# Kernel optimization log

Hardware: AMD Instinct MI355X
Metric: run time of the kernel (lower is better)

The kernel has to match this reference:

```python
import jax, jax.numpy as jnp
import numpy as np
from jax import lax

C = 128
G = 8          # deformable groups
K = 3
KK = K * K
PAD = 1


def conv2d(x, w, pad):
    return lax.conv_general_dilated(
        x, w, window_strides=(1, 1), padding=((pad, pad), (pad, pad)),
        dimension_numbers=('NCHW', 'OIHW', 'NCHW'))


def deform_conv_v2(x, offset, mask, weight, bias):
    """Modulated deformable conv (DCNv2), stride=1, pad=1, dil=1.
    x:[B,C,H,W] offset:[B,2*G*KK,H,W] mask:[B,G*KK,H,W] weight:[O,C,K,K]."""
    B, Cin, H, W = x.shape
    Cg = Cin // G
    # CUDA kernel layout per group: [k0_y, k0_x, k1_y, k1_x, ...]
    off = offset.reshape(B, G, KK, 2, H, W)
    off_y, off_x = off[:, :, :, 0], off[:, :, :, 1]          # [B,G,KK,H,W]
    m = mask.reshape(B, G, KK, H, W)

    kyy, kxx = jnp.meshgrid(jnp.arange(K), jnp.arange(K), indexing='ij')
    kyy = kyy.reshape(KK).astype(x.dtype)
    kxx = kxx.reshape(KK).astype(x.dtype)
    yy = jnp.arange(H, dtype=x.dtype)
    xx = jnp.arange(W, dtype=x.dtype)
    # absolute sampling positions [B,G,KK,H,W]
    py = yy[None, None, None, :, None] - PAD + kyy[None, None, :, None, None] + off_y
    px = xx[None, None, None, None, :] - PAD + kxx[None, None, :, None, None] + off_x

    y0 = jnp.floor(py)
    x0 = jnp.floor(px)
    ly = py - y0
    lx = px - x0

    xg = x.reshape(B, G, Cg, H * W)

    def gather(yi, xi):
        valid = ((yi >= 0) & (yi <= H - 1) & (xi >= 0) & (xi <= W - 1)).astype(x.dtype)
        yc = jnp.clip(yi, 0, H - 1).astype(jnp.int32)
        xc = jnp.clip(xi, 0, W - 1).astype(jnp.int32)
        idx = (yc * W + xc).reshape(B, G, 1, KK * H * W)
        v = jnp.take_along_axis(xg, idx, axis=3).reshape(B, G, Cg, KK, H, W)
        return v * valid[:, :, None]

    val = (gather(y0, x0) * ((1 - ly) * (1 - lx))[:, :, None]
           + gather(y0, x0 + 1) * ((1 - ly) * lx)[:, :, None]
           + gather(y0 + 1, x0) * (ly * (1 - lx))[:, :, None]
           + gather(y0 + 1, x0 + 1) * (ly * lx)[:, :, None])
    val = val * m[:, :, None]                                # modulation

    w = weight.reshape(-1, G, Cg, KK)                        # [O,G,Cg,KK]
    out = jnp.einsum('bgckhw,ogck->bohw', val, w)
    return out + bias[None, :, None, None]


def setup_inputs() -> dict:
    key = jax.random.key(0)
    ks = jax.random.split(key, 7)
    B, H, W = 4, 128, 128
    feat_l = jax.random.normal(ks[0], (B, C, H, W), jnp.float32)
    feat_s = jax.random.normal(ks[1], (B, C, H // 2, W // 2), jnp.float32)
    # 1x1 offset conv (256 -> 128), bias=False
    W_off = jax.random.normal(ks[2], (C, 2 * C, 1, 1), jnp.float32) * (1.0 / np.sqrt(2 * C))
    # conv_offset_mask: 128 -> G*3*KK = 216, 3x3, bias=True (zero-init in practice; small random here)
    W_om = jax.random.normal(ks[3], (G * 3 * KK, C, K, K), jnp.float32) * 0.01
    b_om = jax.random.normal(ks[4], (G * 3 * KK,), jnp.float32) * 0.01
    # DCN weight 128 -> 128, 3x3
    W_dcn = jax.random.normal(ks[5], (C, C, K, K), jnp.float32) * (1.0 / np.sqrt(C * KK))
    b_dcn = jax.random.normal(ks[6], (C,), jnp.float32) * 0.01
    return {'feat_l': feat_l, 'feat_s': feat_s, 'W_off': W_off,
            'W_om': W_om, 'b_om': b_om, 'W_dcn': W_dcn, 'b_dcn': b_dcn}


def reference(feat_l, feat_s, W_off, W_om, b_om, W_dcn, b_dcn):
    B, Cc, H, W = feat_l.shape
    # F.interpolate bilinear align_corners=False == jax.image.resize bilinear
    feat_up = jax.image.resize(feat_s, (B, Cc, H, W), method='bilinear')
    offset_feat = conv2d(jnp.concatenate([feat_l, feat_up * 2], axis=1), W_off, pad=0)
    om = conv2d(offset_feat, W_om, pad=1) + b_om[None, :, None, None]
    o1, o2, mask = jnp.split(om, 3, axis=1)
    offset = jnp.concatenate([o1, o2], axis=1)
    mask = jax.nn.sigmoid(mask)
    feat_align = jax.nn.relu(deform_conv_v2(feat_up, offset, mask, W_dcn, b_dcn))
    return feat_align + feat_l
```

## Files before the change

kernel.cpp:

```cpp
#include <hip/hip_runtime.h>
#include <hip/hip_bf16.h>
#include <math.h>

#define BB 4
#define CC 128
#define HH 128
#define WW 128
#define HWs 16384
#define GG 8
#define OMCH 216

typedef __bf16 bf16_t;
typedef unsigned int u32;
typedef bf16_t bf16x2 __attribute__((ext_vector_type(2)));
typedef bf16_t bf16x4 __attribute__((ext_vector_type(4)));
typedef bf16_t bf16x8 __attribute__((ext_vector_type(8)));
typedef float f32x4 __attribute__((ext_vector_type(4)));

__device__ __forceinline__ float bf2f(u32 hword16) {
    union { u32 u; float f; } t; t.u = hword16 << 16; return t.f;
}

__global__ __launch_bounds__(256) void k_prep(const float* __restrict__ W_off,
                                              const float* __restrict__ W_om,
                                              const float* __restrict__ W_dcn,
                                              bf16_t* __restrict__ wpack1,
                                              bf16_t* __restrict__ wpack,
                                              bf16_t* __restrict__ wpdcn) {
    int idx = blockIdx.x * 256 + threadIdx.x;
    if (idx < 4096) {
        int j = idx;
        int lane = j & 63;
        int rest = j >> 6;
        int ot = rest & 7;
        int ks = rest >> 3;
        int o = ot * 16 + (lane & 15);
        int cbase = ks * 32 + ((lane >> 4) << 3);
        bf16x8 v;
        #pragma unroll
        for (int r = 0; r < 8; ++r) {
            float s = (cbase + r >= 128) ? 2.0f : 1.0f;
            v[r] = (bf16_t)(W_off[o * 256 + cbase + r] * s);
        }
        *((bf16x8*)wpack1 + j) = v;
    } else if (idx < 4096 + 36864) {
        int j = idx - 4096;
        int lane = j & 63;
        int rest = j >> 6;
        int ot = rest & 15;
        int ks = rest >> 4;
        int cblk = ks / 9, tap = ks % 9;
        int o = ot * 16 + (lane & 15);
        int cbase = cblk * 32 + ((lane >> 4) << 3);
        bf16x8 v;
        #pragma unroll
        for (int r = 0; r < 8; ++r) {
            float x = (o < OMCH) ? W_om[((o * 128 + cbase + r) * 9) + tap] : 0.0f;
            v[r] = (bf16_t)x;
        }
        *((bf16x8*)wpack + j) = v;
    } else if (idx < 4096 + 36864 + 20480) {
        int j = idx - 40960;
        int lane = j & 63;
        int rest = j >> 6;
        int ot = rest & 7;
        int gks = rest >> 3;
        int g = gks / 5, ks = gks % 5;
        int o = ot * 16 + (lane & 15);
        int Kbase = ks * 32 + ((lane >> 4) << 3);
        bf16x8 v;
        #pragma unroll
        for (int r = 0; r < 8; ++r) {
            int K = Kbase + r;
            float x = 0.0f;
            if (K < 144) {
                int tap = K >> 4, cpp = K & 15;
                x = W_dcn[((o * 128) + g * 16 + cpp) * 9 + tap];
            }
            v[r] = (bf16_t)x;
        }
        *((bf16x8*)wpdcn + j) = v;
    }
}

__global__ __launch_bounds__(256) void k_upsample(const float* __restrict__ fs,
                                                  bf16_t* __restrict__ fub) {
    int idx = blockIdx.x * 256 + threadIdx.x;
    int i = idx & 63, y = (idx >> 6) & 127, bc = idx >> 13;
    int j = y >> 1;
    int ya, yb; float wya, wyb;
    if (y & 1) { ya = j; yb = (j < 63) ? j + 1 : 63; wya = 0.75f; wyb = 0.25f; }
    else       { ya = (j > 0) ? j - 1 : 0; yb = j;   wya = 0.25f; wyb = 0.75f; }
    int im1 = (i > 0) ? i - 1 : 0;
    int ip1 = (i < 63) ? i + 1 : 63;
    const float* p = fs + (size_t)bc * 4096;
    float am = p[ya * 64 + im1], a0 = p[ya * 64 + i], ap = p[ya * 64 + ip1];
    float bm = p[yb * 64 + im1], b0 = p[yb * 64 + i], bp = p[yb * 64 + ip1];
    float rm = wya * am + wyb * bm;
    float r0 = wya * a0 + wyb * b0;
    float rp = wya * ap + wyb * bp;
    bf16x2 o2;
    o2[0] = (bf16_t)(0.25f * rm + 0.75f * r0);
    o2[1] = (bf16_t)(0.75f * r0 + 0.25f * rp);
    *(bf16x2*)&fub[(size_t)idx * 2] = o2;
}

#define X1LD 264
__global__ __launch_bounds__(256) void k_conv1m(const float* __restrict__ fl,
                                                const bf16_t* __restrict__ fub,
                                                const bf16_t* __restrict__ wp1,
                                                bf16_t* __restrict__ offs) {
    __shared__ __align__(16) bf16_t X[64][X1LD];
    int t = threadIdx.x, lane = t & 63, w = t >> 6;
    int b = blockIdx.x >> 8;
    int pos0 = (blockIdx.x & 255) << 6;
    f32x4 acc[2][4];
    #pragma unroll
    for (int i = 0; i < 2; ++i)
        #pragma unroll
        for (int j = 0; j < 4; ++j)
            acc[i][j] = (f32x4){0.f, 0.f, 0.f, 0.f};
    #pragma unroll 4
    for (int it = 0; it < 32; ++it) {
        int cp = it * 4 + w;
        int c = cp * 2;
        if (c < 128) {
            size_t gb = (size_t)(b * 128 + c) * HWs + pos0 + lane;
            X[lane][c] = (bf16_t)fl[gb];
            X[lane][c + 1] = (bf16_t)fl[gb + HWs];
        } else {
            size_t gb = (size_t)(b * 128 + (c - 128)) * HWs + pos0 + lane;
            X[lane][c] = fub[gb];
            X[lane][c + 1] = fub[gb + HWs];
        }
    }
    __syncthreads();
    #pragma unroll
    for (int ks = 0; ks < 8; ++ks) {
        bf16x8 af[2], bfr[4];
        const bf16x8* wp = (const bf16x8*)wp1 + ((ks * 8 + w * 2) * 64 + lane);
        af[0] = wp[0];
        af[1] = wp[64];
        #pragma unroll
        for (int pi = 0; pi < 4; ++pi)
            bfr[pi] = *(const bf16x8*)&X[pi * 16 + (lane & 15)][ks * 32 + ((lane >> 4) << 3)];
        #pragma unroll
        for (int oi = 0; oi < 2; ++oi)
            #pragma unroll
            for (int pi = 0; pi < 4; ++pi)
                acc[oi][pi] = __builtin_amdgcn_mfma_f32_16x16x32_bf16(af[oi], bfr[pi], acc[oi][pi], 0, 0, 0);
    }
    #pragma unroll
    for (int oi = 0; oi < 2; ++oi) {
        int obase = (w * 2 + oi) * 16 + ((lane >> 4) << 2);
        #pragma unroll
        for (int j = 0; j < 4; ++j) {
            int o = obase + j;
            size_t ob = (size_t)(b * 128 + o) * HWs + pos0 + (lane & 15);
            #pragma unroll
            for (int pi = 0; pi < 4; ++pi)
                offs[ob + pi * 16] = (bf16_t)acc[oi][pi][j];
        }
    }
}

#define X3LD 40
__global__ __launch_bounds__(256) void k_conv3m(const bf16_t* __restrict__ A,
                                                const bf16_t* __restrict__ wpack,
                                                const float* __restrict__ bom,
                                                bf16_t* __restrict__ om) {
    __shared__ __align__(16) bf16_t Xs[3 * 66 * X3LD];
    int t = threadIdx.x;
    int lane = t & 63, w = t >> 6;
    int b = blockIdx.x >> 8;
    int pos0 = (blockIdx.x & 255) << 6;
    int y = pos0 >> 7, x0 = pos0 & 127;
    f32x4 acc[4][4];
    #pragma unroll
    for (int i = 0; i < 4; ++i)
        #pragma unroll
        for (int j = 0; j < 4; ++j)
            acc[i][j] = (f32x4){0.f, 0.f, 0.f, 0.f};

    for (int cblk = 0; cblk < 4; ++cblk) {
        __syncthreads();
        for (int id = t; id < 3168; id += 256) {
            int col = id % 66;
            int rest = id / 66;
            int dy = rest % 3;
            int cp = rest / 3;
            int gy = y - 1 + dy, gx = x0 - 1 + col;
            bf16_t v0 = (bf16_t)0.f, v1 = (bf16_t)0.f;
            if ((unsigned)gy < 128u && (unsigned)gx < 128u) {
                size_t gb = ((size_t)(b * 128 + cblk * 32 + cp * 2) * 128 + gy) * 128 + gx;
                v0 = A[gb];
                v1 = A[gb + HWs];
            }
            int le = (dy * 66 + col) * X3LD + cp * 2;
            Xs[le] = v0;
            Xs[le + 1] = v1;
        }
        __syncthreads();
        #pragma unroll
        for (int tap = 0; tap < 9; ++tap) {
            const int ky = tap / 3, kx = tap % 3;
            bf16x8 af[4], bfr[4];
            const bf16x8* wp = (const bf16x8*)wpack + ((size_t)((cblk * 9 + tap) * 16 + w * 4) * 64 + lane);
            #pragma unroll
            for (int oi = 0; oi < 4; ++oi) af[oi] = wp[oi * 64];
            #pragma unroll
            for (int pi = 0; pi < 4; ++pi) {
                int colb = pi * 16 + (lane & 15) + kx;
                bfr[pi] = *(const bf16x8*)&Xs[(ky * 66 + colb) * X3LD + ((lane >> 4) << 3)];
            }
            #pragma unroll
            for (int oi = 0; oi < 4; ++oi)
                #pragma unroll
                for (int pi = 0; pi < 4; ++pi)
                    acc[oi][pi] = __builtin_amdgcn_mfma_f32_16x16x32_bf16(af[oi], bfr[pi], acc[oi][pi], 0, 0, 0);
        }
    }
    #pragma unroll
    for (int oi = 0; oi < 4; ++oi) {
        int obase = (w * 4 + oi) * 16 + ((lane >> 4) << 2);
        #pragma unroll
        for (int j = 0; j < 4; ++j) {
            int o = obase + j;
            if (o < OMCH) {
                float bv = bom[o];
                size_t ob = (size_t)(b * OMCH + o) * HWs + pos0 + (lane & 15);
                #pragma unroll
                for (int pi = 0; pi < 4; ++pi) {
                    float v = acc[oi][pi][j] + bv;
                    if (o >= 144) v = 1.0f / (1.0f + expf(-v));
                    om[ob + pi * 16] = (bf16_t)v;
                }
            }
        }
    }
}

__global__ __launch_bounds__(512, 4) void k_dcn(const bf16_t* __restrict__ fub,
                                                const bf16_t* __restrict__ om,
                                                const bf16_t* __restrict__ wpd,
                                                const float* __restrict__ bdcn,
                                                const float* __restrict__ fl,
                                                float* __restrict__ outp) {
    __shared__ __align__(16) bf16_t val[2][64][168];
    int t = threadIdx.x;
    int lane = t & 63, w = t >> 6;
    int b = blockIdx.x >> 8;
    int pos0 = (blockIdx.x & 255) << 6;
    int y = pos0 >> 7, x0 = pos0 & 127;
    f32x4 acc[4];
    #pragma unroll
    for (int j = 0; j < 4; ++j) acc[j] = (f32x4){0.f, 0.f, 0.f, 0.f};
    for (int id = t; id < 2 * 64 * 24; id += 512) {
        int bufg = id / 1536, r = id % 1536;
        val[bufg][r / 24][144 + (r % 24)] = (bf16_t)0.0f;
    }

    const bf16_t* omb = om + (size_t)b * OMCH * HWs;
    const bf16_t* fb  = fub + (size_t)b * 128 * HWs;
    size_t sp = (size_t)y * 128 + x0 + lane;

    const int u1gl = (w + 8) / 9, u1tap = (w + 8) % 9;
    const int u2tap = 7 + (w >> 1);
    const int u2c0 = (w & 1) * 8;

    auto process_range = [&](int gl, int g, int tap, float oy, float ox, float m,
                             int ch0, int nch) __attribute__((always_inline)) {
        int ky = tap / 3, kx = tap % 3;
        int x = x0 + lane;
        float py = (float)(y - 1 + ky) + oy;
        float px = (float)(x - 1 + kx) + ox;
        float fy0 = floorf(py), fx0 = floorf(px);
        float ly = py - fy0, lx = px - fx0;
        int y0 = (int)fy0, x0i = (int)fx0;
        float vy0 = ((unsigned)y0 < 128u) ? 1.0f : 0.0f;
        float vy1 = ((unsigned)(y0 + 1) < 128u) ? 1.0f : 0.0f;
        float vx0 = ((unsigned)x0i < 128u) ? 1.0f : 0.0f;
        float vx1 = ((unsigned)(x0i + 1) < 128u) ? 1.0f : 0.0f;
        int yc0 = min(max(y0, 0), 127), yc1 = min(max(y0 + 1, 0), 127);
        int xc0 = min(max(x0i, 0), 127), xc1 = min(max(x0i + 1, 0), 127);
        float pw00 = (1.0f - ly) * (1.0f - lx) * m * vy0 * vx0;
        float pw01 = (1.0f - ly) * lx * m * vy0 * vx1;
        float pw10 = ly * (1.0f - lx) * m * vy1 * vx0;
        float pw11 = ly * lx * m * vy1 * vx1;
        int xr = min(xc0, 126);
        int s0 = xc0 - xr, s1 = xc1 - xr;
        float ax = (s0 ? 0.0f : pw00) + (s1 ? 0.0f : pw01);
        float ay = (s0 ? pw00 : 0.0f) + (s1 ? pw01 : 0.0f);
        float bx = (s0 ? 0.0f : pw10) + (s1 ? 0.0f : pw11);
        float by = (s0 ? pw10 : 0.0f) + (s1 ? pw11 : 0.0f);
        int s = xr & 1;
        int e_lo = yc0 * 128 + xr - s;
        int e_hi = yc1 * 128 + xr - s;
        const bf16_t* bp = fb + (size_t)(g * 16) * HWs;
        for (int cb = 0; cb < nch; cb += 4) {
            u32 alo[4], ahi[4], blo[4], bhi[4];
            #pragma unroll
            for (int c = 0; c < 4; ++c) {
                const bf16_t* p = bp + (size_t)(ch0 + cb + c) * HWs;
                alo[c] = *(const u32*)(p + e_lo);
                ahi[c] = *(const u32*)(p + e_lo + 2);
                blo[c] = *(const u32*)(p + e_hi);
                bhi[c] = *(const u32*)(p + e_hi + 2);
            }
            bf16x4 ov;
            #pragma unroll
            for (int c = 0; c < 4; ++c) {
                u32 ca = s ? ((alo[c] >> 16) | (ahi[c] << 16)) : alo[c];
                u32 cbp = s ? ((blo[c] >> 16) | (bhi[c] << 16)) : blo[c];
                float v = ax * bf2f(ca & 0xffffu) + ay * bf2f(ca >> 16)
                        + bx * bf2f(cbp & 0xffffu) + by * bf2f(cbp >> 16);
                ov[c] = (bf16_t)v;
            }
            *(bf16x4*)&val[gl][lane][tap * 16 + ch0 + cb] = ov;
        }
    };

    float oy0, ox0, m0, oy1, ox1, m1, oy2 = 0.f, ox2 = 0.f, m2 = 0.f;
    {
        int g0 = 0, u1g = u1gl, u2g = 1;
        oy0 = (float)omb[(size_t)(g0 * 18 + w * 2) * HWs + sp];
        ox0 = (float)omb[(size_t)(g0 * 18 + w * 2 + 1) * HWs + sp];
        m0  = (float)omb[(size_t)(144 + g0 * 9 + w) * HWs + sp];
        oy1 = (float)omb[(size_t)(u1g * 18 + u1tap * 2) * HWs + sp];
        ox1 = (float)omb[(size_t)(u1g * 18 + u1tap * 2 + 1) * HWs + sp];
        m1  = (float)omb[(size_t)(144 + u1g * 9 + u1tap) * HWs + sp];
        if (w < 4) {
            oy2 = (float)omb[(size_t)(u2g * 18 + u2tap * 2) * HWs + sp];
            ox2 = (float)omb[(size_t)(u2g * 18 + u2tap * 2 + 1) * HWs + sp];
            m2  = (float)omb[(size_t)(144 + u2g * 9 + u2tap) * HWs + sp];
        }
    }

    for (int gc = 0; gc < 4; ++gc) {
        process_range(0, gc * 2, w, oy0, ox0, m0, 0, 16);
        process_range(u1gl, gc * 2 + u1gl, u1tap, oy1, ox1, m1, 0, 16);
        if (w < 4) process_range(1, gc * 2 + 1, u2tap, oy2, ox2, m2, u2c0, 8);
        if (gc < 3) {
            int g0 = (gc + 1) * 2;
            int u1g = g0 + u1gl, u2g = g0 + 1;
            oy0 = (float)omb[(size_t)(g0 * 18 + w * 2) * HWs + sp];
            ox0 = (float)omb[(size_t)(g0 * 18 + w * 2 + 1) * HWs + sp];
            m0  = (float)omb[(size_t)(144 + g0 * 9 + w) * HWs + sp];
            oy1 = (float)omb[(size_t)(u1g * 18 + u1tap * 2) * HWs + sp];
            ox1 = (float)omb[(size_t)(u1g * 18 + u1tap * 2 + 1) * HWs + sp];
            m1  = (float)omb[(size_t)(144 + u1g * 9 + u1tap) * HWs + sp];
            if (w < 4) {
                oy2 = (float)omb[(size_t)(u2g * 18 + u2tap * 2) * HWs + sp];
                ox2 = (float)omb[(size_t)(u2g * 18 + u2tap * 2 + 1) * HWs + sp];
                m2  = (float)omb[(size_t)(144 + u2g * 9 + u2tap) * HWs + sp];
            }
        }
        __syncthreads();
        #pragma unroll
        for (int gl = 0; gl < 2; ++gl) {
            int g = gc * 2 + gl;
            #pragma unroll
            for (int ks = 0; ks < 5; ++ks) {
                bf16x8 af = *((const bf16x8*)wpd + (((g * 5 + ks) * 8 + w) * 64 + lane));
                #pragma unroll
                for (int pi = 0; pi < 4; ++pi) {
                    bf16x8 bfr = *(const bf16x8*)&val[gl][pi * 16 + (lane & 15)][ks * 32 + ((lane >> 4) << 3)];
                    acc[pi] = __builtin_amdgcn_mfma_f32_16x16x32_bf16(af, bfr, acc[pi], 0, 0, 0);
                }
            }
        }
        __syncthreads();
    }
    #pragma unroll
    for (int j = 0; j < 4; ++j) {
        int o = w * 16 + ((lane >> 4) << 2) + j;
        float bv = bdcn[o];
        size_t base = (size_t)(b * 128 + o) * HWs + pos0 + (lane & 15);
        #pragma unroll
        for (int pi = 0; pi < 4; ++pi) {
            float v = fmaxf(acc[pi][j] + bv, 0.0f) + fl[base + pi * 16];
            outp[base + pi * 16] = v;
        }
    }
}

extern "C" void kernel_launch(void* const* d_in, const int* in_sizes, int n_in,
                              void* d_out, int out_size, void* d_ws, size_t ws_size,
                              hipStream_t stream) {
    const float* feat_l = (const float*)d_in[0];
    const float* feat_s = (const float*)d_in[1];
    const float* W_off  = (const float*)d_in[2];
    const float* W_om   = (const float*)d_in[3];
    const float* b_om   = (const float*)d_in[4];
    const float* W_dcn  = (const float*)d_in[5];
    const float* b_dcn  = (const float*)d_in[6];
    float* out = (float*)d_out;
    float* ws = (float*)d_ws;

    bf16_t* fub    = (bf16_t*)ws;
    bf16_t* offs   = (bf16_t*)(ws + 4194304);
    bf16_t* om     = (bf16_t*)(ws + 8388608);
    bf16_t* wpack1 = (bf16_t*)(ws + 15466496);
    bf16_t* wpack  = (bf16_t*)(ws + 15482880);
    bf16_t* wpdcn  = (bf16_t*)(ws + 15630336);

    k_prep<<<240, 256, 0, stream>>>(W_off, W_om, W_dcn, wpack1, wpack, wpdcn);
    k_upsample<<<16384, 256, 0, stream>>>(feat_s, fub);
    k_conv1m<<<1024, 256, 0, stream>>>(feat_l, fub, wpack1, offs);
    k_conv3m<<<1024, 256, 0, stream>>>(offs, wpack, b_om, om);
    k_dcn<<<1024, 512, 0, stream>>>(fub, om, wpdcn, b_dcn, feat_l, out);
}
```

Measured before the change: 350.9 us.

## Double k_dcn block to 1024 threads and split sampling and MFMA work across 16 waves

```diff
diff --git a/kernel.cpp b/kernel.cpp
--- a/kernel.cpp
+++ b/kernel.cpp
@@ -240,22 +240,22 @@
     }
 }
 
-__global__ __launch_bounds__(512, 4) void k_dcn(const bf16_t* __restrict__ fub,
-                                                const bf16_t* __restrict__ om,
-                                                const bf16_t* __restrict__ wpd,
-                                                const float* __restrict__ bdcn,
-                                                const float* __restrict__ fl,
-                                                float* __restrict__ outp) {
+__global__ __launch_bounds__(1024, 2) void k_dcn(const bf16_t* __restrict__ fub,
+                                                 const bf16_t* __restrict__ om,
+                                                 const bf16_t* __restrict__ wpd,
+                                                 const float* __restrict__ bdcn,
+                                                 const float* __restrict__ fl,
+                                                 float* __restrict__ outp) {
     __shared__ __align__(16) bf16_t val[2][64][168];
     int t = threadIdx.x;
     int lane = t & 63, w = t >> 6;
     int b = blockIdx.x >> 8;
     int pos0 = (blockIdx.x & 255) << 6;
     int y = pos0 >> 7, x0 = pos0 & 127;
-    f32x4 acc[4];
-    #pragma unroll
-    for (int j = 0; j < 4; ++j) acc[j] = (f32x4){0.f, 0.f, 0.f, 0.f};
-    for (int id = t; id < 2 * 64 * 24; id += 512) {
+    f32x4 acc[2];
+    acc[0] = (f32x4){0.f, 0.f, 0.f, 0.f};
+    acc[1] = (f32x4){0.f, 0.f, 0.f, 0.f};
+    for (int id = t; id < 2 * 64 * 24; id += 1024) {
         int bufg = id / 1536, r = id % 1536;
         val[bufg][r / 24][144 + (r % 24)] = (bf16_t)0.0f;
     }
@@ -264,9 +264,12 @@
     const bf16_t* fb  = fub + (size_t)b * 128 * HWs;
     size_t sp = (size_t)y * 128 + x0 + lane;
 
-    const int u1gl = (w + 8) / 9, u1tap = (w + 8) % 9;
-    const int u2tap = 7 + (w >> 1);
-    const int u2c0 = (w & 1) * 8;
+    const int u0gl = (w >= 9) ? 1 : 0;
+    const int u0tap = w - 9 * u0gl;
+    const int uXtap = (w < 4) ? 7 : 8;
+    const int uXc0 = (w & 3) * 4;
+    const int ot = w >> 1;
+    const int ph = w & 1;
 
     auto process_range = [&](int gl, int g, int tap, float oy, float ox, float m,
                              int ch0, int nch) __attribute__((always_inline)) {
@@ -320,39 +323,33 @@
         }
     };
 
-    float oy0, ox0, m0, oy1, ox1, m1, oy2 = 0.f, ox2 = 0.f, m2 = 0.f;
+    float oy0, ox0, m0, oyX = 0.f, oxX = 0.f, mX = 0.f;
     {
-        int g0 = 0, u1g = u1gl, u2g = 1;
-        oy0 = (float)omb[(size_t)(g0 * 18 + w * 2) * HWs + sp];
-        ox0 = (float)omb[(size_t)(g0 * 18 + w * 2 + 1) * HWs + sp];
-        m0  = (float)omb[(size_t)(144 + g0 * 9 + w) * HWs + sp];
-        oy1 = (float)omb[(size_t)(u1g * 18 + u1tap * 2) * HWs + sp];
-        ox1 = (float)omb[(size_t)(u1g * 18 + u1tap * 2 + 1) * HWs + sp];
-        m1  = (float)omb[(size_t)(144 + u1g * 9 + u1tap) * HWs + sp];
-        if (w < 4) {
-            oy2 = (float)omb[(size_t)(u2g * 18 + u2tap * 2) * HWs + sp];
-            ox2 = (float)omb[(size_t)(u2g * 18 + u2tap * 2 + 1) * HWs + sp];
-            m2  = (float)omb[(size_t)(144 + u2g * 9 + u2tap) * HWs + sp];
+        int g0 = u0gl;
+        oy0 = (float)omb[(size_t)(g0 * 18 + u0tap * 2) * HWs + sp];
+        ox0 = (float)omb[(size_t)(g0 * 18 + u0tap * 2 + 1) * HWs + sp];
+        m0  = (float)omb[(size_t)(144 + g0 * 9 + u0tap) * HWs + sp];
+        if (w < 8) {
+            int gX = 1;
+            oyX = (float)omb[(size_t)(gX * 18 + uXtap * 2) * HWs + sp];
+            oxX = (float)omb[(size_t)(gX * 18 + uXtap * 2 + 1) * HWs + sp];
+            mX  = (float)omb[(size_t)(144 + gX * 9 + uXtap) * HWs + sp];
         }
     }
 
     for (int gc = 0; gc < 4; ++gc) {
-        process_range(0, gc * 2, w, oy0, ox0, m0, 0, 16);
-        process_range(u1gl, gc * 2 + u1gl, u1tap, oy1, ox1, m1, 0, 16);
-        if (w < 4) process_range(1, gc * 2 + 1, u2tap, oy2, ox2, m2, u2c0, 8);
+        process_range(u0gl, gc * 2 + u0gl, u0tap, oy0, ox0, m0, 0, 16);
+        if (w < 8) process_range(1, gc * 2 + 1, uXtap, oyX, oxX, mX, uXc0, 4);
         if (gc < 3) {
-            int g0 = (gc + 1) * 2;
-            int u1g = g0 + u1gl, u2g = g0 + 1;
-            oy0 = (float)omb[(size_t)(g0 * 18 + w * 2) * HWs + sp];
-            ox0 = (float)omb[(size_t)(g0 * 18 + w * 2 + 1) * HWs + sp];
-            m0  = (float)omb[(size_t)(144 + g0 * 9 + w) * HWs + sp];
-            oy1 = (float)omb[(size_t)(u1g * 18 + u1tap * 2) * HWs + sp];
-            ox1 = (float)omb[(size_t)(u1g * 18 + u1tap * 2 + 1) * HWs + sp];
-            m1  = (float)omb[(size_t)(144 + u1g * 9 + u1tap) * HWs + sp];
-            if (w < 4) {
-                oy2 = (float)omb[(size_t)(u2g * 18 + u2tap * 2) * HWs + sp];
-                ox2 = (float)omb[(size_t)(u2g * 18 + u2tap * 2 + 1) * HWs + sp];
-                m2  = (float)omb[(size_t)(144 + u2g * 9 + u2tap) * HWs + sp];
+            int g0 = (gc + 1) * 2 + u0gl;
+            oy0 = (float)omb[(size_t)(g0 * 18 + u0tap * 2) * HWs + sp];
+            ox0 = (float)omb[(size_t)(g0 * 18 + u0tap * 2 + 1) * HWs + sp];
+            m0  = (float)omb[(size_t)(144 + g0 * 9 + u0tap) * HWs + sp];
+            if (w < 8) {
+                int gX = (gc + 1) * 2 + 1;
+                oyX = (float)omb[(size_t)(gX * 18 + uXtap * 2) * HWs + sp];
+                oxX = (float)omb[(size_t)(gX * 18 + uXtap * 2 + 1) * HWs + sp];
+                mX  = (float)omb[(size_t)(144 + gX * 9 + uXtap) * HWs + sp];
             }
         }
         __syncthreads();
@@ -361,11 +358,12 @@
             int g = gc * 2 + gl;
             #pragma unroll
             for (int ks = 0; ks < 5; ++ks) {
-                bf16x8 af = *((const bf16x8*)wpd + (((g * 5 + ks) * 8 + w) * 64 + lane));
+                bf16x8 af = *((const bf16x8*)wpd + (((g * 5 + ks) * 8 + ot) * 64 + lane));
                 #pragma unroll
-                for (int pi = 0; pi < 4; ++pi) {
+                for (int pl = 0; pl < 2; ++pl) {
+                    int pi = ph * 2 + pl;
                     bf16x8 bfr = *(const bf16x8*)&val[gl][pi * 16 + (lane & 15)][ks * 32 + ((lane >> 4) << 3)];
-                    acc[pi] = __builtin_amdgcn_mfma_f32_16x16x32_bf16(af, bfr, acc[pi], 0, 0, 0);
+                    acc[pl] = __builtin_amdgcn_mfma_f32_16x16x32_bf16(af, bfr, acc[pl], 0, 0, 0);
                 }
             }
         }
@@ -373,12 +371,13 @@
     }
     #pragma unroll
     for (int j = 0; j < 4; ++j) {
-        int o = w * 16 + ((lane >> 4) << 2) + j;
+        int o = ot * 16 + ((lane >> 4) << 2) + j;
         float bv = bdcn[o];
         size_t base = (size_t)(b * 128 + o) * HWs + pos0 + (lane & 15);
         #pragma unroll
-        for (int pi = 0; pi < 4; ++pi) {
-            float v = fmaxf(acc[pi][j] + bv, 0.0f) + fl[base + pi * 16];
+        for (int pl = 0; pl < 2; ++pl) {
+            int pi = ph * 2 + pl;
+            float v = fmaxf(acc[pl][j] + bv, 0.0f) + fl[base + pi * 16];
             outp[base + pi * 16] = v;
         }
     }
@@ -408,5 +407,5 @@
     k_upsample<<<16384, 256, 0, stream>>>(feat_s, fub);
     k_conv1m<<<1024, 256, 0, stream>>>(feat_l, fub, wpack1, offs);
     k_conv3m<<<1024, 256, 0, stream>>>(offs, wpack, b_om, om);
-    k_dcn<<<1024, 512, 0, stream>>>(fub, om, wpdcn, b_dcn, feat_l, out);
-}
+    k_dcn<<<1024, 1024, 0, stream>>>(fub, om, wpdcn, b_dcn, feat_l, out);
+}
```

Result: slower. 368.2 us (+4.9%).
